# Optimization experiments

Measured on AMD Instinct MI355X. Metric: run time of the kernel, lower is better.

The kernel has to match this reference:

```python
import jax, jax.numpy as jnp
import numpy as np

B, H, N, D = 4, 16, 2048, 64

def setup_inputs() -> dict:
    key = jax.random.key(0)
    kq, kk, kv = jax.random.split(key, 3)
    q = jax.random.normal(kq, (B, H, N, D), dtype=jnp.float32)
    k = jax.random.normal(kk, (B, H, N, D), dtype=jnp.float32)
    v = jax.random.normal(kv, (B, H, N, D), dtype=jnp.float32)
    return {"q": q, "k": k, "v": v}

def reference(q, k, v):
    scale = q.shape[-1] ** -0.5
    # sim: [b, h, i, j]
    sim = jnp.einsum('bhid,bhjd->bhij', q, k) * scale
    attn = jax.nn.softmax(sim, axis=-1)  # dropout p=0.0 -> identity
    out = jnp.einsum('bhij,bhjd->bhid', attn, v)
    return out
```

## Files before the change

### kernel.cpp

```cpp
#include <hip/hip_runtime.h>
#include <stdint.h>


#define NSEQ 2048
#define DH   64
#define BHN  64
#define NIT  32

typedef short bf16x8 __attribute__((ext_vector_type(8)));
typedef float f32x4  __attribute__((ext_vector_type(4)));
typedef float f32x16 __attribute__((ext_vector_type(16)));

__device__ __forceinline__ uint16_t f2bf(float x) {
    uint32_t u = __builtin_bit_cast(uint32_t, x);
    return (uint16_t)((u + 0x7fffu + ((u >> 16) & 1u)) >> 16);
}
__device__ __forceinline__ uint32_t pk2(float a, float b) {
    return (uint32_t)f2bf(a) | ((uint32_t)f2bf(b) << 16);
}

__global__ __launch_bounds__(256) void prepass(const float* __restrict__ K,
                                               const float* __restrict__ V,
                                               uint16_t* __restrict__ F) {
    __shared__ float T0[64 * 68];
    __shared__ float T1[64 * 68];
    const int b = blockIdx.x, bh = b >> 5, kt = b & 31, t = threadIdx.x;
    const size_t gbase = ((size_t)bh * NSEQ + (size_t)kt * 64) * DH;
    const int n = t >> 2, d0 = (t & 3) * 16;
    #pragma unroll
    for (int i = 0; i < 4; ++i) {
        *(float4*)&T0[n * 68 + d0 + i * 4] = *(const float4*)(K + gbase + n * 64 + d0 + i * 4);
        *(float4*)&T1[n * 68 + d0 + i * 4] = *(const float4*)(V + gbase + n * 64 + d0 + i * 4);
    }
    __syncthreads();
    uint16_t* out = F + (size_t)(bh * 32 + kt) * 8192;
    #pragma unroll
    for (int p = 0; p < 4; ++p) {
        const int e = p * 256 + t, c = e >> 6, l = e & 63;
        const int ll = l & 31, hh = l >> 5;
        float f[8];
        if (c < 8) {
            const int row = (c >> 2) * 32 + ll;
            const int col = hh * 8 + (c & 3) * 16;
            #pragma unroll
            for (int j = 0; j < 8; ++j) f[j] = T0[row * 68 + col + j];
        } else {
            const int cc = c - 8, ktg = cc >> 1;
            const int d = (cc & 1) * 32 + ll;
            #pragma unroll
            for (int j = 0; j < 8; ++j) {
                const int i = hh * 8 + j;
                const int s = (i & 3) + 8 * ((i >> 2) & 1) + 4 * ((i >> 3) & 1);
                f[j] = T1[(ktg * 16 + s) * 68 + d];
            }
        }
        uint4 o = make_uint4(pk2(f[0], f[1]), pk2(f[2], f[3]),
                             pk2(f[4], f[5]), pk2(f[6], f[7]));
        *(uint4*)(out + (size_t)c * 512 + l * 8) = o;
    }
}

__device__ __forceinline__ void load_q(const float* qp, float qscale, bf16x8 (&dst)[4]) {
    #pragma unroll
    for (int k2 = 0; k2 < 4; ++k2) {
        float4 a = *(const float4*)(qp + k2 * 16);
        float4 c = *(const float4*)(qp + k2 * 16 + 4);
        union { uint32_t u[4]; bf16x8 v; } pk;
        pk.u[0] = pk2(a.x * qscale, a.y * qscale);
        pk.u[1] = pk2(a.z * qscale, a.w * qscale);
        pk.u[2] = pk2(c.x * qscale, c.y * qscale);
        pk.u[3] = pk2(c.z * qscale, c.w * qscale);
        dst[k2] = pk.v;
    }
}

__device__ __forceinline__ void tile_mtj(const uint4 (&kc)[4], const uint4 (&vc)[4],
                                         const bf16x8 (&qfn)[4],
                                         f32x16& o0, f32x16& o1, float& lsn) {
    f32x16 s = {};
    #pragma unroll
    for (int k2 = 0; k2 < 4; ++k2)
        s = __builtin_amdgcn_mfma_f32_32x32x16_bf16(
            __builtin_bit_cast(bf16x8, kc[k2]), qfn[k2], s, 0, 0, 0);
    bf16x8 pf0, pf1;
    float g0, g1;
    {
        union { uint32_t u[4]; bf16x8 v; } pp;
        float e[8];
        #pragma unroll
        for (int t2 = 0; t2 < 4; ++t2) {
            e[2 * t2]     = __builtin_amdgcn_exp2f(s[2 * t2]);
            e[2 * t2 + 1] = __builtin_amdgcn_exp2f(s[2 * t2 + 1]);
            pp.u[t2] = __builtin_amdgcn_perm(
                __builtin_bit_cast(uint32_t, e[2 * t2 + 1]),
                __builtin_bit_cast(uint32_t, e[2 * t2]), 0x07060302u);
        }
        g0 = ((e[0] + e[1]) + (e[2] + e[3])) + ((e[4] + e[5]) + (e[6] + e[7]));
        pf0 = pp.v;
    }
    {
        union { uint32_t u[4]; bf16x8 v; } pp;
        float e[8];
        #pragma unroll
        for (int t2 = 0; t2 < 4; ++t2) {
            e[2 * t2]     = __builtin_amdgcn_exp2f(s[8 + 2 * t2]);
            e[2 * t2 + 1] = __builtin_amdgcn_exp2f(s[8 + 2 * t2 + 1]);
            pp.u[t2] = __builtin_amdgcn_perm(
                __builtin_bit_cast(uint32_t, e[2 * t2 + 1]),
                __builtin_bit_cast(uint32_t, e[2 * t2]), 0x07060302u);
        }
        g1 = ((e[0] + e[1]) + (e[2] + e[3])) + ((e[4] + e[5]) + (e[6] + e[7]));
        pf1 = pp.v;
    }
    lsn += g0 + g1;
    o0 = __builtin_amdgcn_mfma_f32_32x32x16_bf16(
        pf0, __builtin_bit_cast(bf16x8, vc[0]), o0, 0, 0, 0);
    o0 = __builtin_amdgcn_mfma_f32_32x32x16_bf16(
        pf1, __builtin_bit_cast(bf16x8, vc[2]), o0, 0, 0, 0);
    o1 = __builtin_amdgcn_mfma_f32_32x32x16_bf16(
        pf0, __builtin_bit_cast(bf16x8, vc[1]), o1, 0, 0, 0);
    o1 = __builtin_amdgcn_mfma_f32_32x32x16_bf16(
        pf1, __builtin_bit_cast(bf16x8, vc[3]), o1, 0, 0, 0);
}

__device__ __forceinline__ void ep_write(float* Ob, int row0,
                                         const f32x16& a0, const f32x16& a1,
                                         float lt, int l31, int h) {
    const float rinv = 1.0f / lt;
    const int rib = __builtin_bit_cast(int, rinv);
    #pragma unroll
    for (int rg = 0; rg < 16; ++rg) {
        const int il = (rg & 3) + 8 * (rg >> 2) + 4 * h;
        const float inv = __builtin_bit_cast(float,
            __builtin_amdgcn_ds_bpermute(il * 4, rib));
        const int row = row0 + il;
        Ob[(size_t)row * DH + l31]      = a0[rg] * inv;
        Ob[(size_t)row * DH + 32 + l31] = a1[rg] * inv;
    }
}

__device__ __forceinline__ void stage_tile(uint16_t* sb, const uint16_t* ft,
                                           int w, int lane) {
    #pragma unroll
    for (int j = 0; j < 4; ++j) {
        const int c = w * 4 + j;
        __builtin_amdgcn_global_load_lds(
            (const __attribute__((address_space(1))) void*)(ft + (size_t)c * 512 + (size_t)lane * 8),
            (__attribute__((address_space(3))) void*)(sb + c * 512),
            16, 0, 0);
    }
}

__global__ __launch_bounds__(256, 4) void attn_main(const float* __restrict__ Qg,
                                                    const uint16_t* __restrict__ F,
                                                    float* __restrict__ Og) {
    __shared__ __align__(16) uint16_t SB[2][8192];
    const int tid = threadIdx.x;
    const int w = tid >> 6, lane = tid & 63;
    const int l31 = lane & 31, h = lane >> 5;
    const int idx = blockIdx.x;
    const int bh = (idx & 7) * 8 + ((idx >> 3) & 7);
    const int qt2 = idx >> 6;

    const float qscale = 0.125f * 1.44269504f;
    bf16x8 qf[4];
    load_q(Qg + ((size_t)bh * NSEQ + (size_t)(qt2 * 128 + w * 32 + l31)) * DH + h * 8,
           qscale, qf);

    f32x16 oa0 = {}, oa1 = {};
    float ls = 0.0f;

    const uint16_t* fbase = F + (size_t)bh * 32 * 8192;

    stage_tile(&SB[0][0], fbase, w, lane);
    #pragma unroll 1
    for (int kt = 0; kt < NIT; ++kt) {
        if (kt + 1 < NIT) {
            stage_tile(&SB[(kt + 1) & 1][0], fbase + (size_t)(kt + 1) * 8192, w, lane);
            asm volatile("s_waitcnt vmcnt(4)" ::: "memory");
        } else {
            asm volatile("s_waitcnt vmcnt(0)" ::: "memory");
        }
        __builtin_amdgcn_s_barrier();
        __builtin_amdgcn_sched_barrier(0);
        const uint16_t* sb = &SB[kt & 1][0];
        uint4 kcl[4], kch[4], vcl[4], vch[4];
        #pragma unroll
        for (int c = 0; c < 4; ++c) kcl[c] = *(const uint4*)(sb + (c) * 512 + lane * 8);
        #pragma unroll
        for (int c = 0; c < 4; ++c) kch[c] = *(const uint4*)(sb + (4 + c) * 512 + lane * 8);
        #pragma unroll
        for (int c = 0; c < 4; ++c) vcl[c] = *(const uint4*)(sb + (8 + c) * 512 + lane * 8);
        #pragma unroll
        for (int c = 0; c < 4; ++c) vch[c] = *(const uint4*)(sb + (12 + c) * 512 + lane * 8);
        tile_mtj(kcl, vcl, qf, oa0, oa1, ls);
        tile_mtj(kch, vch, qf, oa0, oa1, ls);
        __builtin_amdgcn_sched_barrier(0);
        __builtin_amdgcn_s_barrier();
    }

    float lt = ls + __shfl_xor(ls, 32);
    float* Ob = Og + (size_t)bh * NSEQ * DH;
    ep_write(Ob, qt2 * 128 + w * 32, oa0, oa1, lt, l31, h);
}

#define LDS_S 72
#define NWAVE 4
#define BN    64
__global__ __launch_bounds__(256) void attn_fwd_fb(const float* __restrict__ Qg,
                                                   const float* __restrict__ Kg,
                                                   const float* __restrict__ Vg,
                                                   float* __restrict__ Og) {
    __shared__ short KsF[BN * LDS_S];
    __shared__ short VtsF[DH * LDS_S];
    __shared__ short PsF[NWAVE * 16 * LDS_S];
    const int tid = threadIdx.x;
    const int wave = tid >> 6, lane = tid & 63, quad = lane >> 4, l16 = lane & 15;
    const int bh = blockIdx.x >> 5, qtf = blockIdx.x & 31;
    const size_t base = (size_t)bh * NSEQ * DH;
    const float* Qb = Qg + base; const float* Kbf = Kg + base;
    const float* Vb = Vg + base; float* Ob = Og + base;
    const float qscale = 0.125f * 1.44269504f;
    bf16x8 qfrag[2];
    {
        const int qrow = qtf * 64 + wave * 16 + l16;
        const float* qp = Qb + (size_t)qrow * DH + quad * 8;
        #pragma unroll
        for (int c = 0; c < 2; ++c) {
            float4 x = *(const float4*)(qp + 32 * c);
            float4 y = *(const float4*)(qp + 32 * c + 4);
            union { uint16_t u[8]; bf16x8 v; } pk;
            pk.u[0]=f2bf(x.x*qscale); pk.u[1]=f2bf(x.y*qscale);
            pk.u[2]=f2bf(x.z*qscale); pk.u[3]=f2bf(x.w*qscale);
            pk.u[4]=f2bf(y.x*qscale); pk.u[5]=f2bf(y.y*qscale);
            pk.u[6]=f2bf(y.z*qscale); pk.u[7]=f2bf(y.w*qscale);
            qfrag[c] = pk.v;
        }
    }
    f32x4 o[4] = {};
    float m_i[4], l_i[4];
    #pragma unroll
    for (int r = 0; r < 4; ++r) { m_i[r] = -1e30f; l_i[r] = 0.0f; }
    const int kr0 = tid >> 4, kd0 = (tid & 15) * 4;
    const int vp = (tid & 31) * 2, vd0 = (tid >> 5) * 8;
    #pragma unroll 1
    for (int kt = 0; kt < NSEQ / BN; ++kt) {
        __syncthreads();
        {
            const float* kbase = Kbf + (size_t)kt * BN * DH;
            #pragma unroll
            for (int jj = 0; jj < 4; ++jj) {
                const int row = kr0 + jj * 16;
                float4 x = *(const float4*)(kbase + (size_t)row * DH + kd0);
                union { uint16_t u[4]; uint64_t ll; } pk;
                pk.u[0]=f2bf(x.x); pk.u[1]=f2bf(x.y); pk.u[2]=f2bf(x.z); pk.u[3]=f2bf(x.w);
                *(uint64_t*)&KsF[row * LDS_S + kd0] = pk.ll;
            }
        }
        {
            const float* v0 = Vb + (size_t)(kt * BN + vp) * DH + vd0;
            const float* v1 = v0 + DH;
            float4 a0 = *(const float4*)(v0); float4 a1 = *(const float4*)(v0 + 4);
            float4 b0 = *(const float4*)(v1); float4 b1 = *(const float4*)(v1 + 4);
            float av[8] = {a0.x,a0.y,a0.z,a0.w,a1.x,a1.y,a1.z,a1.w};
            float bv[8] = {b0.x,b0.y,b0.z,b0.w,b1.x,b1.y,b1.z,b1.w};
            #pragma unroll
            for (int i = 0; i < 8; ++i)
                *(uint32_t*)&VtsF[(vd0 + i) * LDS_S + vp] = pk2(av[i], bv[i]);
        }
        __syncthreads();
        f32x4 s[4] = {};
        #pragma unroll
        for (int c = 0; c < 2; ++c)
            #pragma unroll
            for (int n = 0; n < 4; ++n) {
                bf16x8 kfr = *(const bf16x8*)&KsF[(n * 16 + l16) * LDS_S + quad * 8 + 32 * c];
                s[n] = __builtin_amdgcn_mfma_f32_16x16x32_bf16(qfrag[c], kfr, s[n], 0, 0, 0);
            }
        float rmax[4];
        #pragma unroll
        for (int r = 0; r < 4; ++r)
            rmax[r] = fmaxf(fmaxf(s[0][r], s[1][r]), fmaxf(s[2][r], s[3][r]));
        #pragma unroll
        for (int off = 1; off < 16; off <<= 1)
            #pragma unroll
            for (int r = 0; r < 4; ++r)
                rmax[r] = fmaxf(rmax[r], __shfl_xor(rmax[r], off, 64));
        float alpha[4], rsum[4];
        #pragma unroll
        for (int r = 0; r < 4; ++r) {
            float mn = fmaxf(m_i[r], rmax[r]);
            alpha[r] = __builtin_amdgcn_exp2f(m_i[r] - mn);
            m_i[r] = mn; rsum[r] = 0.0f;
        }
        #pragma unroll
        for (int n = 0; n < 4; ++n)
            #pragma unroll
            for (int r = 0; r < 4; ++r) {
                float p = __builtin_amdgcn_exp2f(s[n][r] - m_i[r]);
                rsum[r] += p;
                PsF[(wave * 16 + quad * 4 + r) * LDS_S + n * 16 + l16] = (short)f2bf(p);
            }
        #pragma unroll
        for (int off = 1; off < 16; off <<= 1)
            #pragma unroll
            for (int r = 0; r < 4; ++r)
                rsum[r] += __shfl_xor(rsum[r], off, 64);
        #pragma unroll
        for (int r = 0; r < 4; ++r) l_i[r] = l_i[r] * alpha[r] + rsum[r];
        #pragma unroll
        for (int n = 0; n < 4; ++n)
            #pragma unroll
            for (int r = 0; r < 4; ++r) o[n][r] *= alpha[r];
        #pragma unroll
        for (int c = 0; c < 2; ++c) {
            bf16x8 pfr = *(const bf16x8*)&PsF[(wave * 16 + l16) * LDS_S + quad * 8 + 32 * c];
            #pragma unroll
            for (int n = 0; n < 4; ++n) {
                bf16x8 vfr = *(const bf16x8*)&VtsF[(n * 16 + l16) * LDS_S + quad * 8 + 32 * c];
                o[n] = __builtin_amdgcn_mfma_f32_16x16x32_bf16(pfr, vfr, o[n], 0, 0, 0);
            }
        }
    }
    float inv[4];
    #pragma unroll
    for (int r = 0; r < 4; ++r) inv[r] = 1.0f / l_i[r];
    const int orow0 = qtf * 64 + wave * 16 + quad * 4;
    #pragma unroll
    for (int n = 0; n < 4; ++n)
        #pragma unroll
        for (int r = 0; r < 4; ++r)
            Ob[(size_t)(orow0 + r) * DH + n * 16 + l16] = o[n][r] * inv[r];
}

extern "C" void kernel_launch(void* const* d_in, const int* in_sizes, int n_in,
                              void* d_out, int out_size, void* d_ws, size_t ws_size,
                              hipStream_t stream) {
    (void)in_sizes; (void)n_in; (void)out_size;
    const float* q = (const float*)d_in[0];
    const float* k = (const float*)d_in[1];
    const float* v = (const float*)d_in[2];
    float* out = (float*)d_out;
    const size_t need = (size_t)BHN * 32 * 16384;
    if (ws_size >= need) {
        uint16_t* fbuf = (uint16_t*)d_ws;
        prepass<<<dim3(BHN * 32), dim3(256), 0, stream>>>(k, v, fbuf);
        attn_main<<<dim3(1024), dim3(256), 0, stream>>>(q, fbuf, out);
    } else {
        attn_fwd_fb<<<dim3(BHN * 32), dim3(256), 0, stream>>>(q, k, v, out);
    }
}
```

Baseline: 201.9 us.

## Process two 32-row query tiles per wave and deepen K/V prefetch to four buffers

Each wave now handles 64 query rows (two Q fragment sets) against the same K/V tile loaded from LDS, halving the grid to 512 blocks and doubling reuse of each staged K/V tile. The LDS ring grows from two to four buffers with a two-tile-ahead prefetch, and the trailing barrier is removed. The goal is less global and LDS traffic per unit of MFMA work and better latency hiding. In exchange it uses more registers and LDS (launch bounds drop to 2 blocks per CU) and launches fewer blocks, which may leave some CUs underused on mi355x.

```diff
diff --git a/kernel.cpp b/kernel.cpp
--- a/kernel.cpp
+++ b/kernel.cpp
@@ -151,57 +151,74 @@
     }
 }
 
-__global__ __launch_bounds__(256, 4) void attn_main(const float* __restrict__ Qg,
+__global__ __launch_bounds__(256, 2) void attn_main(const float* __restrict__ Qg,
                                                     const uint16_t* __restrict__ F,
                                                     float* __restrict__ Og) {
-    __shared__ __align__(16) uint16_t SB[2][8192];
+    __shared__ __align__(16) uint16_t SB[4][8192];
     const int tid = threadIdx.x;
     const int w = tid >> 6, lane = tid & 63;
     const int l31 = lane & 31, h = lane >> 5;
     const int idx = blockIdx.x;
     const int bh = (idx & 7) * 8 + ((idx >> 3) & 7);
-    const int qt2 = idx >> 6;
+    const int qt = idx >> 6;
 
     const float qscale = 0.125f * 1.44269504f;
-    bf16x8 qf[4];
-    load_q(Qg + ((size_t)bh * NSEQ + (size_t)(qt2 * 128 + w * 32 + l31)) * DH + h * 8,
-           qscale, qf);
-
-    f32x16 oa0 = {}, oa1 = {};
-    float ls = 0.0f;
+    bf16x8 qf0[4], qf1[4];
+    {
+        const float* qb = Qg + ((size_t)bh * NSEQ +
+                                (size_t)(qt * 256 + w * 64 + l31)) * DH + h * 8;
+        load_q(qb, qscale, qf0);
+        load_q(qb + 32 * DH, qscale, qf1);
+    }
+
+    f32x16 oa00 = {}, oa01 = {}, oa10 = {}, oa11 = {};
+    float ls0 = 0.0f, ls1 = 0.0f;
 
     const uint16_t* fbase = F + (size_t)bh * 32 * 8192;
 
     stage_tile(&SB[0][0], fbase, w, lane);
+    stage_tile(&SB[1][0], fbase + 8192, w, lane);
+
     #pragma unroll 1
     for (int kt = 0; kt < NIT; ++kt) {
-        if (kt + 1 < NIT) {
-            stage_tile(&SB[(kt + 1) & 1][0], fbase + (size_t)(kt + 1) * 8192, w, lane);
+        if (kt + 2 < NIT) {
+            stage_tile(&SB[(kt + 2) & 3][0], fbase + (size_t)(kt + 2) * 8192, w, lane);
+            asm volatile("s_waitcnt vmcnt(8)" ::: "memory");
+        } else if (kt + 2 == NIT) {
             asm volatile("s_waitcnt vmcnt(4)" ::: "memory");
         } else {
             asm volatile("s_waitcnt vmcnt(0)" ::: "memory");
         }
         __builtin_amdgcn_s_barrier();
         __builtin_amdgcn_sched_barrier(0);
-        const uint16_t* sb = &SB[kt & 1][0];
-        uint4 kcl[4], kch[4], vcl[4], vch[4];
-        #pragma unroll
-        for (int c = 0; c < 4; ++c) kcl[c] = *(const uint4*)(sb + (c) * 512 + lane * 8);
-        #pragma unroll
-        for (int c = 0; c < 4; ++c) kch[c] = *(const uint4*)(sb + (4 + c) * 512 + lane * 8);
-        #pragma unroll
-        for (int c = 0; c < 4; ++c) vcl[c] = *(const uint4*)(sb + (8 + c) * 512 + lane * 8);
-        #pragma unroll
-        for (int c = 0; c < 4; ++c) vch[c] = *(const uint4*)(sb + (12 + c) * 512 + lane * 8);
-        tile_mtj(kcl, vcl, qf, oa0, oa1, ls);
-        tile_mtj(kch, vch, qf, oa0, oa1, ls);
+        const uint16_t* sb = &SB[kt & 3][0];
+        {
+            uint4 kc[4], vc[4];
+            #pragma unroll
+            for (int c = 0; c < 4; ++c) kc[c] = *(const uint4*)(sb + (c) * 512 + lane * 8);
+            #pragma unroll
+            for (int c = 0; c < 4; ++c) vc[c] = *(const uint4*)(sb + (8 + c) * 512 + lane * 8);
+            tile_mtj(kc, vc, qf0, oa00, oa01, ls0);
+            tile_mtj(kc, vc, qf1, oa10, oa11, ls1);
+        }
+        {
+            uint4 kc[4], vc[4];
+            #pragma unroll
+            for (int c = 0; c < 4; ++c) kc[c] = *(const uint4*)(sb + (4 + c) * 512 + lane * 8);
+            #pragma unroll
+            for (int c = 0; c < 4; ++c) vc[c] = *(const uint4*)(sb + (12 + c) * 512 + lane * 8);
+            tile_mtj(kc, vc, qf0, oa00, oa01, ls0);
+            tile_mtj(kc, vc, qf1, oa10, oa11, ls1);
+        }
         __builtin_amdgcn_sched_barrier(0);
-        __builtin_amdgcn_s_barrier();
-    }
-
-    float lt = ls + __shfl_xor(ls, 32);
+    }
+
+    float lt0 = ls0 + __shfl_xor(ls0, 32);
+    float lt1 = ls1 + __shfl_xor(ls1, 32);
     float* Ob = Og + (size_t)bh * NSEQ * DH;
-    ep_write(Ob, qt2 * 128 + w * 32, oa0, oa1, lt, l31, h);
+    const int row0 = qt * 256 + w * 64;
+    ep_write(Ob, row0,      oa00, oa01, lt0, l31, h);
+    ep_write(Ob, row0 + 32, oa10, oa11, lt1, l31, h);
 }
 
 #define LDS_S 72
@@ -345,7 +362,7 @@
     if (ws_size >= need) {
         uint16_t* fbuf = (uint16_t*)d_ws;
         prepass<<<dim3(BHN * 32), dim3(256), 0, stream>>>(k, v, fbuf);
-        attn_main<<<dim3(1024), dim3(256), 0, stream>>>(q, fbuf, out);
+        attn_main<<<dim3(512), dim3(256), 0, stream>>>(q, fbuf, out);
     } else {
         attn_fwd_fb<<<dim3(BHN * 32), dim3(256), 0, stream>>>(q, k, v, out);
     }
```

New measurement: 194.4 us. -3.7%, faster.
